# Optimization experiments

Measured on AMD Instinct MI355X. Metric: run time of the kernel, lower is better.

Reference implementation:

```python
import jax, jax.numpy as jnp
import numpy as np
from jax import lax

VOCAB, EMB, HID, NCLS, BATCH, SEQ = 32000, 512, 512, 8, 64, 512


def setup_inputs() -> dict:
    key = jax.random.key(0)
    ks = jax.random.split(key, 12)
    s = 0.05
    return {
        "x": jax.random.randint(ks[0], (BATCH, SEQ), 0, VOCAB),
        "emb": jax.random.normal(ks[1], (VOCAB, EMB), jnp.float32) * s,
        "W_ih0": jax.random.normal(ks[2], (HID, EMB), jnp.float32) * s,
        "W_hh0": jax.random.normal(ks[3], (HID, HID), jnp.float32) * s,
        "b_ih0": jax.random.normal(ks[4], (HID,), jnp.float32) * s,
        "b_hh0": jax.random.normal(ks[5], (HID,), jnp.float32) * s,
        "W_ih1": jax.random.normal(ks[6], (HID, HID), jnp.float32) * s,
        "W_hh1": jax.random.normal(ks[7], (HID, HID), jnp.float32) * s,
        "b_ih1": jax.random.normal(ks[8], (HID,), jnp.float32) * s,
        "b_hh1": jax.random.normal(ks[9], (HID,), jnp.float32) * s,
        "fc_W": jax.random.normal(ks[10], (NCLS, HID), jnp.float32) * s,
        "fc_b": jax.random.normal(ks[11], (NCLS,), jnp.float32) * s,
    }


def _rnn_layer(inp, W_ih, W_hh, b_ih, b_hh):
    # inp: [B, S, F]; tanh RNN, batch_first. Precompute input projection once.
    pre = jnp.einsum('bsf,hf->bsh', inp, W_ih) + b_ih + b_hh  # [B,S,H]
    B = inp.shape[0]
    H = W_hh.shape[0]
    h0 = jnp.zeros((B, H), inp.dtype)

    def step(h, p_t):  # p_t: [B,H]
        h = jnp.tanh(p_t + h @ W_hh.T)
        return h, h

    hT, ys = lax.scan(step, h0, pre.transpose(1, 0, 2))  # scan over time
    return ys.transpose(1, 0, 2), hT  # outputs [B,S,H], last hidden [B,H]


def reference(x, emb, W_ih0, W_hh0, b_ih0, b_hh0, W_ih1, W_hh1, b_ih1, b_hh1, fc_W, fc_b):
    xe = emb[x]  # [B,S,E] embedding lookup
    out0, _ = _rnn_layer(xe, W_ih0, W_hh0, b_ih0, b_hh0)
    _, h1 = _rnn_layer(out0, W_ih1, W_hh1, b_ih1, b_hh1)  # hidden[-1]
    return h1 @ fc_W.T + fc_b  # [B, n_class]
```

## Files before the change

kernel.cpp:

```cpp
#include <hip/hip_runtime.h>
#include <stdint.h>


#define BB 64
#define SS 512
#define HH 512

typedef short bf16x8 __attribute__((ext_vector_type(8)));
typedef float f32x4 __attribute__((ext_vector_type(4)));
typedef int i32x4 __attribute__((ext_vector_type(4)));
typedef unsigned int u32;
typedef u32 u32x2 __attribute__((ext_vector_type(2)));

__device__ __forceinline__ unsigned short f2bf(float f) {
  uint32_t u = __builtin_bit_cast(uint32_t, f);
  u += 0x7FFFu + ((u >> 16) & 1u);
  return (unsigned short)(u >> 16);
}
__device__ __forceinline__ float bf2f(unsigned short h) {
  uint32_t u = ((uint32_t)h) << 16;
  return __builtin_bit_cast(float, u);
}
__device__ __forceinline__ int pack2(unsigned short a, unsigned short b) {
  return (int)(unsigned int)a | ((int)(unsigned int)b << 16);
}
__device__ __forceinline__ u32 hipack(u32 a, u32 b) {
  return (a >> 16) | (b & 0xFFFF0000u);
}
__device__ __forceinline__ u32 lopack(u32 a, u32 b) {
  return (a & 0xFFF8u) | ((b & 0xFFF8u) << 16);
}
__device__ __forceinline__ bool tag4(i32x4 v, u32 t) {
  u32 m = (((u32)v[0] ^ t) | ((u32)v[1] ^ t) | ((u32)v[2] ^ t) | ((u32)v[3] ^ t)) & 7u;
  return m == 0u;
}
__device__ __forceinline__ float fast_tanh(float v) {
  float a = __builtin_fabsf(v);
  float e = __expf(-2.0f * a);
  float t = (1.0f - e) / (1.0f + e);
  return __builtin_copysignf(t, v);
}

#define UC_LOAD4(dst, ptr) \
  asm volatile("global_load_dwordx4 %0, %1, off sc0 sc1" : "=v"(dst) : "v"(ptr))
#define UC_LOAD1(dst, ptr) \
  asm volatile("global_load_dword %0, %1, off sc0 sc1" : "=v"(dst) : "v"(ptr))
#define UC_STORE2(ptr, v) \
  asm volatile("global_store_dwordx2 %0, %1, off sc0 sc1" ::"v"(ptr), "v"(v) : "memory")

__global__ __launch_bounds__(512, 2) void k_rnn(
    const int* __restrict__ x, const float* __restrict__ emb,
    const float* __restrict__ Wih0, const float* __restrict__ Whh0,
    const float* __restrict__ bih0, const float* __restrict__ bhh0,
    const float* __restrict__ Wih1, const float* __restrict__ Whh1,
    const float* __restrict__ bih1, const float* __restrict__ bhh1,
    u32* __restrict__ hsl) {
  const int tid = threadIdx.x;
  const int bid = blockIdx.x;
  const int layer = bid >> 5;
  const int lb = bid & 31;
  const int bg = lb >> 3;
  const int c = lb & 7;
  const int wid = tid >> 6;
  const int lane = tid & 63;
  const int kq = wid >> 1;
  const int nh = wid & 1;

  __shared__ __align__(16) unsigned short s_in0[16 * 512];
  __shared__ __align__(16) unsigned short s_Hhi[16 * 512];
  __shared__ __align__(16) unsigned short s_Hlo[16 * 512];
  __shared__ __align__(16) float s_part[4 * 16 * 64];

  const float* Wih = layer ? Wih1 : Wih0;
  const float* Whh = layer ? Whh1 : Whh0;
  const float* bi = layer ? bih1 : bih0;
  const float* bh = layer ? bhh1 : bhh0;

  bf16x8 wih[2][4], whhh[2][4], whhl[2][4];
  {
    const int r16 = lane & 15, kg = lane >> 4;
#pragma unroll
    for (int nt = 0; nt < 2; ++nt) {
#pragma unroll
      for (int kt = 0; kt < 4; ++kt) {
        int row = c * 64 + nh * 32 + nt * 16 + r16;
        int k0 = kq * 128 + kt * 32 + kg * 8;
        const float* p = Wih + row * 512 + k0;
        bf16x8 v;
#pragma unroll
        for (int j = 0; j < 8; ++j) v[j] = (short)f2bf(p[j]);
        wih[nt][kt] = v;
        const float* q = Whh + row * 512 + k0;
        bf16x8 vh, vl;
#pragma unroll
        for (int j = 0; j < 8; ++j) {
          float f = q[j];
          unsigned short h = f2bf(f);
          vh[j] = (short)h;
          vl[j] = (short)f2bf(f - bf2f(h));
        }
        whhh[nt][kt] = vh;
        whhl[nt][kt] = vl;
      }
    }
  }
  float biasv0, biasv1;
  {
    int na = (tid & 31) * 2;
    biasv0 = bi[c * 64 + na] + bh[c * 64 + na];
    biasv1 = bi[c * 64 + na + 1] + bh[c * 64 + na + 1];
  }

  const int r_st = tid >> 5;
  const int ch = tid & 31;

  float4 pf0, pf1, pf2, pf3;
  if (layer == 0) {
    int rid = x[(bg * 16 + r_st) * SS + 0];
    const float4* ep = (const float4*)(emb + (size_t)rid * 512 + ch * 16);
    pf0 = ep[0]; pf1 = ep[1]; pf2 = ep[2]; pf3 = ep[3];
  }

  for (int s = 1; s <= SS; ++s) {
    const u32 exp_h = (u32)((s - 1) & 7);
    const u32* ph = hsl +
        (((size_t)layer * 4 + ((s - 1) & 3)) * 64 + bg * 16 + r_st) * 512 + ch * 16;

    if (layer == 0) {
      i32x4 v0, v1;
      v0[0] = pack2(f2bf(pf0.x), f2bf(pf0.y));
      v0[1] = pack2(f2bf(pf0.z), f2bf(pf0.w));
      v0[2] = pack2(f2bf(pf1.x), f2bf(pf1.y));
      v0[3] = pack2(f2bf(pf1.z), f2bf(pf1.w));
      v1[0] = pack2(f2bf(pf2.x), f2bf(pf2.y));
      v1[1] = pack2(f2bf(pf2.z), f2bf(pf2.w));
      v1[2] = pack2(f2bf(pf3.x), f2bf(pf3.y));
      v1[3] = pack2(f2bf(pf3.z), f2bf(pf3.w));
      *(i32x4*)(s_in0 + r_st * 512 + (((2 * ch) ^ (r_st & 7)) << 3)) = v0;
      *(i32x4*)(s_in0 + r_st * 512 + (((2 * ch + 1) ^ (r_st & 7)) << 3)) = v1;
      if (s < SS) {
        int rid = x[(bg * 16 + r_st) * SS + s];
        const float4* ep = (const float4*)(emb + (size_t)rid * 512 + ch * 16);
        pf0 = ep[0]; pf1 = ep[1]; pf2 = ep[2]; pf3 = ep[3];
      }
    } else {
      i32x4 i0 = {0, 0, 0, 0}, i1 = {0, 0, 0, 0}, i2 = {0, 0, 0, 0}, i3 = {0, 0, 0, 0};
      const u32 exp_i = (u32)(s & 7);
      const u32* pi =
          hsl + (((size_t)(s & 3)) * 64 + bg * 16 + r_st) * 512 + ch * 16;
      while (true) {
        UC_LOAD4(i0, pi);
        UC_LOAD4(i1, pi + 4);
        UC_LOAD4(i2, pi + 8);
        UC_LOAD4(i3, pi + 12);
        asm volatile("s_waitcnt vmcnt(0)"
                     : "+v"(i0), "+v"(i1), "+v"(i2), "+v"(i3)::"memory");
        bool ok = tag4(i0, exp_i) && tag4(i1, exp_i) && tag4(i2, exp_i) &&
                  tag4(i3, exp_i);
        if (__all(ok)) break;
      }
      i32x4 A0 = {(int)hipack(i0[0], i0[1]), (int)hipack(i0[2], i0[3]),
                  (int)hipack(i1[0], i1[1]), (int)hipack(i1[2], i1[3])};
      i32x4 A1 = {(int)hipack(i2[0], i2[1]), (int)hipack(i2[2], i2[3]),
                  (int)hipack(i3[0], i3[1]), (int)hipack(i3[2], i3[3])};
      *(i32x4*)(s_in0 + r_st * 512 + (((2 * ch) ^ (r_st & 7)) << 3)) = A0;
      *(i32x4*)(s_in0 + r_st * 512 + (((2 * ch + 1) ^ (r_st & 7)) << 3)) = A1;
    }
    __syncthreads();

    f32x4 acc0 = {0.f, 0.f, 0.f, 0.f};
    f32x4 acc1 = {0.f, 0.f, 0.f, 0.f};
    {
      const int r16 = lane & 15, kg = lane >> 4;
#pragma unroll
      for (int kt = 0; kt < 4; ++kt) {
        int k8 = kq * 16 + kt * 4 + kg;
        bf16x8 ain = __builtin_bit_cast(
            bf16x8, *(const i32x4*)(s_in0 + r16 * 512 + ((k8 ^ (r16 & 7)) << 3)));
        acc0 = __builtin_amdgcn_mfma_f32_16x16x32_bf16(ain, wih[0][kt], acc0, 0, 0, 0);
        acc1 = __builtin_amdgcn_mfma_f32_16x16x32_bf16(ain, wih[1][kt], acc1, 0, 0, 0);
      }
    }

    if (s > 1) {
      i32x4 h0 = {0, 0, 0, 0}, h1 = {0, 0, 0, 0}, h2 = {0, 0, 0, 0}, h3 = {0, 0, 0, 0};
      if (layer == 0) {
        const bool need_bp = (s > 4) && (tid < 8);
        const u32 exp_bp = (u32)((s - 4) & 7);
        const u32* pbp = hsl + ((size_t)(4 + ((s - 4) & 3)) * 64 + bg * 16) * 512 +
                         (tid < 8 ? tid * 64 : 0);
        while (true) {
          u32 bpw = 0;
          UC_LOAD4(h0, ph);
          UC_LOAD4(h1, ph + 4);
          UC_LOAD4(h2, ph + 8);
          UC_LOAD4(h3, ph + 12);
          UC_LOAD1(bpw, pbp);
          asm volatile("s_waitcnt vmcnt(0)"
                       : "+v"(h0), "+v"(h1), "+v"(h2), "+v"(h3), "+v"(bpw)::"memory");
          bool ok = tag4(h0, exp_h) && tag4(h1, exp_h) && tag4(h2, exp_h) &&
                    tag4(h3, exp_h) && (!need_bp || ((bpw & 7u) == exp_bp));
          if (__all(ok)) break;
        }
      } else {
        while (true) {
          UC_LOAD4(h0, ph);
          UC_LOAD4(h1, ph + 4);
          UC_LOAD4(h2, ph + 8);
          UC_LOAD4(h3, ph + 12);
          asm volatile("s_waitcnt vmcnt(0)"
                       : "+v"(h0), "+v"(h1), "+v"(h2), "+v"(h3)::"memory");
          bool ok = tag4(h0, exp_h) && tag4(h1, exp_h) && tag4(h2, exp_h) &&
                    tag4(h3, exp_h);
          if (__all(ok)) break;
        }
      }
      i32x4 A0 = {(int)hipack(h0[0], h0[1]), (int)hipack(h0[2], h0[3]),
                  (int)hipack(h1[0], h1[1]), (int)hipack(h1[2], h1[3])};
      i32x4 A1 = {(int)hipack(h2[0], h2[1]), (int)hipack(h2[2], h2[3]),
                  (int)hipack(h3[0], h3[1]), (int)hipack(h3[2], h3[3])};
      i32x4 B0 = {(int)lopack(h0[0], h0[1]), (int)lopack(h0[2], h0[3]),
                  (int)lopack(h1[0], h1[1]), (int)lopack(h1[2], h1[3])};
      i32x4 B1v = {(int)lopack(h2[0], h2[1]), (int)lopack(h2[2], h2[3]),
                   (int)lopack(h3[0], h3[1]), (int)lopack(h3[2], h3[3])};
      *(i32x4*)(s_Hhi + r_st * 512 + (((2 * ch) ^ (r_st & 7)) << 3)) = A0;
      *(i32x4*)(s_Hhi + r_st * 512 + (((2 * ch + 1) ^ (r_st & 7)) << 3)) = A1;
      *(i32x4*)(s_Hlo + r_st * 512 + (((2 * ch) ^ (r_st & 7)) << 3)) = B0;
      *(i32x4*)(s_Hlo + r_st * 512 + (((2 * ch + 1) ^ (r_st & 7)) << 3)) = B1v;
    }
    __syncthreads();

    {
      const int r16 = lane & 15, kg = lane >> 4;
      if (s > 1) {
#pragma unroll
        for (int kt = 0; kt < 4; ++kt) {
          int k8 = kq * 16 + kt * 4 + kg;
          bf16x8 ahi = __builtin_bit_cast(
              bf16x8, *(const i32x4*)(s_Hhi + r16 * 512 + ((k8 ^ (r16 & 7)) << 3)));
          bf16x8 alo = __builtin_bit_cast(
              bf16x8, *(const i32x4*)(s_Hlo + r16 * 512 + ((k8 ^ (r16 & 7)) << 3)));
          acc0 = __builtin_amdgcn_mfma_f32_16x16x32_bf16(ahi, whhh[0][kt], acc0, 0, 0, 0);
          acc0 = __builtin_amdgcn_mfma_f32_16x16x32_bf16(ahi, whhl[0][kt], acc0, 0, 0, 0);
          acc0 = __builtin_amdgcn_mfma_f32_16x16x32_bf16(alo, whhh[0][kt], acc0, 0, 0, 0);
          acc1 = __builtin_amdgcn_mfma_f32_16x16x32_bf16(ahi, whhh[1][kt], acc1, 0, 0, 0);
          acc1 = __builtin_amdgcn_mfma_f32_16x16x32_bf16(ahi, whhl[1][kt], acc1, 0, 0, 0);
          acc1 = __builtin_amdgcn_mfma_f32_16x16x32_bf16(alo, whhh[1][kt], acc1, 0, 0, 0);
        }
      }
#pragma unroll
      for (int j = 0; j < 4; ++j) {
        int m = kg * 4 + j;
        int xr = (m >> 2) & 3;
        int n0i = nh * 32 + 0 * 16 + r16;
        int n1i = nh * 32 + 1 * 16 + r16;
        s_part[kq * 1024 + m * 64 + (n0i ^ (xr << 4))] = acc0[j];
        s_part[kq * 1024 + m * 64 + (n1i ^ (xr << 4))] = acc1[j];
      }
    }
    __syncthreads();

    {
      int m = tid >> 5, na = (tid & 31) * 2;
      int xr = (m >> 2) & 3;
      float v0 = biasv0, v1 = biasv1;
#pragma unroll
      for (int q2 = 0; q2 < 4; ++q2) {
        const float2* sp =
            (const float2*)(s_part + q2 * 1024 + m * 64 + (na ^ (xr << 4)));
        float2 t = *sp;
        v0 += t.x;
        v1 += t.y;
      }
      v0 = fast_tanh(v0);
      v1 = fast_tanh(v1);
      unsigned short a0 = f2bf(v0), a1 = f2bf(v1);
      unsigned short b0 = f2bf(v0 - bf2f(a0)), b1 = f2bf(v1 - bf2f(a1));
      u32 tag = (u32)(s & 7);
      u32x2 wv;
      wv[0] = ((u32)a0 << 16) | ((u32)b0 & 0xFFF8u) | tag;
      wv[1] = ((u32)a1 << 16) | ((u32)b1 & 0xFFF8u) | tag;
      u32* dst = hsl + (((size_t)layer * 4 + (s & 3)) * 64 + bg * 16 + m) * 512 +
                 c * 64 + na;
      UC_STORE2(dst, wv);
    }
  }
}

__global__ void k_fc(const u32* __restrict__ h1w, const float* __restrict__ fcW,
                     const float* __restrict__ fcb, float* __restrict__ out) {
  int i = threadIdx.x;
  int b = i >> 3, cc = i & 7;
  float acc = fcb[cc];
  const u32* ph = h1w + b * 512;
  const float* pw = fcW + cc * 512;
  for (int k = 0; k < 512; k += 4) {
    int4 w4 = *(const int4*)(ph + k);
    float4 wv = *(const float4*)(pw + k);
    acc += (bf2f((unsigned short)((u32)w4.x >> 16)) +
            bf2f((unsigned short)((u32)w4.x & 0xFFF8u))) * wv.x;
    acc += (bf2f((unsigned short)((u32)w4.y >> 16)) +
            bf2f((unsigned short)((u32)w4.y & 0xFFF8u))) * wv.y;
    acc += (bf2f((unsigned short)((u32)w4.z >> 16)) +
            bf2f((unsigned short)((u32)w4.z & 0xFFF8u))) * wv.z;
    acc += (bf2f((unsigned short)((u32)w4.w >> 16)) +
            bf2f((unsigned short)((u32)w4.w & 0xFFF8u))) * wv.w;
  }
  out[b * 8 + cc] = acc;
}

extern "C" void kernel_launch(void* const* d_in, const int* in_sizes, int n_in,
                              void* d_out, int out_size, void* d_ws, size_t ws_size,
                              hipStream_t stream) {
  const int* x = (const int*)d_in[0];
  const float* emb = (const float*)d_in[1];
  const float* Wih0 = (const float*)d_in[2];
  const float* Whh0 = (const float*)d_in[3];
  const float* bih0 = (const float*)d_in[4];
  const float* bhh0 = (const float*)d_in[5];
  const float* Wih1 = (const float*)d_in[6];
  const float* Whh1 = (const float*)d_in[7];
  const float* bih1 = (const float*)d_in[8];
  const float* bhh1 = (const float*)d_in[9];
  const float* fcW = (const float*)d_in[10];
  const float* fcb = (const float*)d_in[11];

  u32* hsl = (u32*)d_ws;

  hipMemsetAsync(hsl, 0, (size_t)2 * 4 * 64 * 512 * 4, stream);
  hipLaunchKernelGGL(k_rnn, dim3(64), dim3(512), 0, stream, x, emb, Wih0, Whh0,
                     bih0, bhh0, Wih1, Whh1, bih1, bhh1, hsl);
  hipLaunchKernelGGL(k_fc, dim3(1), dim3(512), 0, stream,
                     hsl + (size_t)4 * 64 * 512, fcW, fcb, (float*)d_out);
}
```

Measured before the change: 2.071 ms.

## Split input staging and hidden polling across warp halves, drop a barrier

Result: faster. 1.748 ms (-15.6%).

```diff
diff --git a/kernel.cpp b/kernel.cpp
--- a/kernel.cpp
+++ b/kernel.cpp
@@ -48,7 +48,7 @@
 #define UC_STORE2(ptr, v) \
   asm volatile("global_store_dwordx2 %0, %1, off sc0 sc1" ::"v"(ptr), "v"(v) : "memory")
 
-__global__ __launch_bounds__(512, 2) void k_rnn(
+__global__ __launch_bounds__(512, 1) void k_rnn(
     const int* __restrict__ x, const float* __restrict__ emb,
     const float* __restrict__ Wih0, const float* __restrict__ Whh0,
     const float* __restrict__ bih0, const float* __restrict__ bhh0,
@@ -65,6 +65,9 @@
   const int lane = tid & 63;
   const int kq = wid >> 1;
   const int nh = wid & 1;
+  const int gt = tid & 255;
+  const int gr = gt >> 4;
+  const int gch = gt & 15;
 
   __shared__ __align__(16) unsigned short s_in0[16 * 512];
   __shared__ __align__(16) unsigned short s_Hhi[16 * 512];
@@ -111,60 +114,165 @@
     biasv1 = bi[c * 64 + na + 1] + bh[c * 64 + na + 1];
   }
 
-  const int r_st = tid >> 5;
-  const int ch = tid & 31;
-
-  float4 pf0, pf1, pf2, pf3;
-  if (layer == 0) {
-    int rid = x[(bg * 16 + r_st) * SS + 0];
-    const float4* ep = (const float4*)(emb + (size_t)rid * 512 + ch * 16);
-    pf0 = ep[0]; pf1 = ep[1]; pf2 = ep[2]; pf3 = ep[3];
+  float4 pf0, pf1, pf2, pf3, pf4, pf5, pf6, pf7;
+  if (layer == 0 && wid < 4) {
+    int rid = x[(bg * 16 + gr) * SS + 0];
+    const float4* ep = (const float4*)(emb + (size_t)rid * 512);
+    pf0 = ep[2 * gch + 0];  pf1 = ep[2 * gch + 1];
+    pf2 = ep[2 * gch + 32]; pf3 = ep[2 * gch + 33];
+    pf4 = ep[2 * gch + 64]; pf5 = ep[2 * gch + 65];
+    pf6 = ep[2 * gch + 96]; pf7 = ep[2 * gch + 97];
   }
 
   for (int s = 1; s <= SS; ++s) {
     const u32 exp_h = (u32)((s - 1) & 7);
-    const u32* ph = hsl +
-        (((size_t)layer * 4 + ((s - 1) & 3)) * 64 + bg * 16 + r_st) * 512 + ch * 16;
-
-    if (layer == 0) {
-      i32x4 v0, v1;
-      v0[0] = pack2(f2bf(pf0.x), f2bf(pf0.y));
-      v0[1] = pack2(f2bf(pf0.z), f2bf(pf0.w));
-      v0[2] = pack2(f2bf(pf1.x), f2bf(pf1.y));
-      v0[3] = pack2(f2bf(pf1.z), f2bf(pf1.w));
-      v1[0] = pack2(f2bf(pf2.x), f2bf(pf2.y));
-      v1[1] = pack2(f2bf(pf2.z), f2bf(pf2.w));
-      v1[2] = pack2(f2bf(pf3.x), f2bf(pf3.y));
-      v1[3] = pack2(f2bf(pf3.z), f2bf(pf3.w));
-      *(i32x4*)(s_in0 + r_st * 512 + (((2 * ch) ^ (r_st & 7)) << 3)) = v0;
-      *(i32x4*)(s_in0 + r_st * 512 + (((2 * ch + 1) ^ (r_st & 7)) << 3)) = v1;
-      if (s < SS) {
-        int rid = x[(bg * 16 + r_st) * SS + s];
-        const float4* ep = (const float4*)(emb + (size_t)rid * 512 + ch * 16);
-        pf0 = ep[0]; pf1 = ep[1]; pf2 = ep[2]; pf3 = ep[3];
+
+    if (wid < 4) {
+      if (layer == 0) {
+        {
+          i32x4 v;
+          v[0] = pack2(f2bf(pf0.x), f2bf(pf0.y));
+          v[1] = pack2(f2bf(pf0.z), f2bf(pf0.w));
+          v[2] = pack2(f2bf(pf1.x), f2bf(pf1.y));
+          v[3] = pack2(f2bf(pf1.z), f2bf(pf1.w));
+          *(i32x4*)(s_in0 + gr * 512 + (((gch + 0) ^ (gr & 7)) << 3)) = v;
+          v[0] = pack2(f2bf(pf2.x), f2bf(pf2.y));
+          v[1] = pack2(f2bf(pf2.z), f2bf(pf2.w));
+          v[2] = pack2(f2bf(pf3.x), f2bf(pf3.y));
+          v[3] = pack2(f2bf(pf3.z), f2bf(pf3.w));
+          *(i32x4*)(s_in0 + gr * 512 + (((gch + 16) ^ (gr & 7)) << 3)) = v;
+          v[0] = pack2(f2bf(pf4.x), f2bf(pf4.y));
+          v[1] = pack2(f2bf(pf4.z), f2bf(pf4.w));
+          v[2] = pack2(f2bf(pf5.x), f2bf(pf5.y));
+          v[3] = pack2(f2bf(pf5.z), f2bf(pf5.w));
+          *(i32x4*)(s_in0 + gr * 512 + (((gch + 32) ^ (gr & 7)) << 3)) = v;
+          v[0] = pack2(f2bf(pf6.x), f2bf(pf6.y));
+          v[1] = pack2(f2bf(pf6.z), f2bf(pf6.w));
+          v[2] = pack2(f2bf(pf7.x), f2bf(pf7.y));
+          v[3] = pack2(f2bf(pf7.z), f2bf(pf7.w));
+          *(i32x4*)(s_in0 + gr * 512 + (((gch + 48) ^ (gr & 7)) << 3)) = v;
+        }
+        if (s < SS) {
+          int rid = x[(bg * 16 + gr) * SS + s];
+          const float4* ep = (const float4*)(emb + (size_t)rid * 512);
+          pf0 = ep[2 * gch + 0];  pf1 = ep[2 * gch + 1];
+          pf2 = ep[2 * gch + 32]; pf3 = ep[2 * gch + 33];
+          pf4 = ep[2 * gch + 64]; pf5 = ep[2 * gch + 65];
+          pf6 = ep[2 * gch + 96]; pf7 = ep[2 * gch + 97];
+        }
+      } else {
+        i32x4 w0 = {0,0,0,0}, w1 = {0,0,0,0}, w2 = {0,0,0,0}, w3 = {0,0,0,0};
+        i32x4 w4 = {0,0,0,0}, w5 = {0,0,0,0}, w6 = {0,0,0,0}, w7 = {0,0,0,0};
+        const u32 exp_i = (u32)(s & 7);
+        const u32* pib =
+            hsl + (((size_t)(s & 3)) * 64 + bg * 16 + gr) * 512;
+        while (true) {
+          UC_LOAD4(w0, pib + 8 * gch + 0);
+          UC_LOAD4(w1, pib + 8 * gch + 4);
+          UC_LOAD4(w2, pib + 8 * gch + 128);
+          UC_LOAD4(w3, pib + 8 * gch + 132);
+          UC_LOAD4(w4, pib + 8 * gch + 256);
+          UC_LOAD4(w5, pib + 8 * gch + 260);
+          UC_LOAD4(w6, pib + 8 * gch + 384);
+          UC_LOAD4(w7, pib + 8 * gch + 388);
+          asm volatile("s_waitcnt vmcnt(0)"
+                       : "+v"(w0), "+v"(w1), "+v"(w2), "+v"(w3), "+v"(w4),
+                         "+v"(w5), "+v"(w6), "+v"(w7)::"memory");
+          bool ok = tag4(w0, exp_i) && tag4(w1, exp_i) && tag4(w2, exp_i) &&
+                    tag4(w3, exp_i) && tag4(w4, exp_i) && tag4(w5, exp_i) &&
+                    tag4(w6, exp_i) && tag4(w7, exp_i);
+          if (__all(ok)) break;
+        }
+        i32x4 A;
+        A[0] = (int)hipack(w0[0], w0[1]); A[1] = (int)hipack(w0[2], w0[3]);
+        A[2] = (int)hipack(w1[0], w1[1]); A[3] = (int)hipack(w1[2], w1[3]);
+        *(i32x4*)(s_in0 + gr * 512 + (((gch + 0) ^ (gr & 7)) << 3)) = A;
+        A[0] = (int)hipack(w2[0], w2[1]); A[1] = (int)hipack(w2[2], w2[3]);
+        A[2] = (int)hipack(w3[0], w3[1]); A[3] = (int)hipack(w3[2], w3[3]);
+        *(i32x4*)(s_in0 + gr * 512 + (((gch + 16) ^ (gr & 7)) << 3)) = A;
+        A[0] = (int)hipack(w4[0], w4[1]); A[1] = (int)hipack(w4[2], w4[3]);
+        A[2] = (int)hipack(w5[0], w5[1]); A[3] = (int)hipack(w5[2], w5[3]);
+        *(i32x4*)(s_in0 + gr * 512 + (((gch + 32) ^ (gr & 7)) << 3)) = A;
+        A[0] = (int)hipack(w6[0], w6[1]); A[1] = (int)hipack(w6[2], w6[3]);
+        A[2] = (int)hipack(w7[0], w7[1]); A[3] = (int)hipack(w7[2], w7[3]);
+        *(i32x4*)(s_in0 + gr * 512 + (((gch + 48) ^ (gr & 7)) << 3)) = A;
       }
     } else {
-      i32x4 i0 = {0, 0, 0, 0}, i1 = {0, 0, 0, 0}, i2 = {0, 0, 0, 0}, i3 = {0, 0, 0, 0};
-      const u32 exp_i = (u32)(s & 7);
-      const u32* pi =
-          hsl + (((size_t)(s & 3)) * 64 + bg * 16 + r_st) * 512 + ch * 16;
-      while (true) {
-        UC_LOAD4(i0, pi);
-        UC_LOAD4(i1, pi + 4);
-        UC_LOAD4(i2, pi + 8);
-        UC_LOAD4(i3, pi + 12);
-        asm volatile("s_waitcnt vmcnt(0)"
-                     : "+v"(i0), "+v"(i1), "+v"(i2), "+v"(i3)::"memory");
-        bool ok = tag4(i0, exp_i) && tag4(i1, exp_i) && tag4(i2, exp_i) &&
-                  tag4(i3, exp_i);
-        if (__all(ok)) break;
-      }
-      i32x4 A0 = {(int)hipack(i0[0], i0[1]), (int)hipack(i0[2], i0[3]),
-                  (int)hipack(i1[0], i1[1]), (int)hipack(i1[2], i1[3])};
-      i32x4 A1 = {(int)hipack(i2[0], i2[1]), (int)hipack(i2[2], i2[3]),
-                  (int)hipack(i3[0], i3[1]), (int)hipack(i3[2], i3[3])};
-      *(i32x4*)(s_in0 + r_st * 512 + (((2 * ch) ^ (r_st & 7)) << 3)) = A0;
-      *(i32x4*)(s_in0 + r_st * 512 + (((2 * ch + 1) ^ (r_st & 7)) << 3)) = A1;
+      if (s > 1) {
+        i32x4 w0 = {0,0,0,0}, w1 = {0,0,0,0}, w2 = {0,0,0,0}, w3 = {0,0,0,0};
+        i32x4 w4 = {0,0,0,0}, w5 = {0,0,0,0}, w6 = {0,0,0,0}, w7 = {0,0,0,0};
+        const u32* phb = hsl +
+            (((size_t)layer * 4 + ((s - 1) & 3)) * 64 + bg * 16 + gr) * 512;
+        if (layer == 0) {
+          const bool need_bp = (s > 4) && (gt < 8);
+          const u32 exp_bp = (u32)((s - 4) & 7);
+          const u32* pbp = hsl + ((size_t)(4 + ((s - 4) & 3)) * 64 + bg * 16) * 512 +
+                           (gt < 8 ? gt * 64 : 0);
+          while (true) {
+            u32 bpw = 0;
+            UC_LOAD4(w0, phb + 8 * gch + 0);
+            UC_LOAD4(w1, phb + 8 * gch + 4);
+            UC_LOAD4(w2, phb + 8 * gch + 128);
+            UC_LOAD4(w3, phb + 8 * gch + 132);
+            UC_LOAD4(w4, phb + 8 * gch + 256);
+            UC_LOAD4(w5, phb + 8 * gch + 260);
+            UC_LOAD4(w6, phb + 8 * gch + 384);
+            UC_LOAD4(w7, phb + 8 * gch + 388);
+            UC_LOAD1(bpw, pbp);
+            asm volatile("s_waitcnt vmcnt(0)"
+                         : "+v"(w0), "+v"(w1), "+v"(w2), "+v"(w3), "+v"(w4),
+                           "+v"(w5), "+v"(w6), "+v"(w7), "+v"(bpw)::"memory");
+            bool ok = tag4(w0, exp_h) && tag4(w1, exp_h) && tag4(w2, exp_h) &&
+                      tag4(w3, exp_h) && tag4(w4, exp_h) && tag4(w5, exp_h) &&
+                      tag4(w6, exp_h) && tag4(w7, exp_h) &&
+                      (!need_bp || ((bpw & 7u) == exp_bp));
+            if (__all(ok)) break;
+          }
+        } else {
+          while (true) {
+            UC_LOAD4(w0, phb + 8 * gch + 0);
+            UC_LOAD4(w1, phb + 8 * gch + 4);
+            UC_LOAD4(w2, phb + 8 * gch + 128);
+            UC_LOAD4(w3, phb + 8 * gch + 132);
+            UC_LOAD4(w4, phb + 8 * gch + 256);
+            UC_LOAD4(w5, phb + 8 * gch + 260);
+            UC_LOAD4(w6, phb + 8 * gch + 384);
+            UC_LOAD4(w7, phb + 8 * gch + 388);
+            asm volatile("s_waitcnt vmcnt(0)"
+                         : "+v"(w0), "+v"(w1), "+v"(w2), "+v"(w3), "+v"(w4),
+                           "+v"(w5), "+v"(w6), "+v"(w7)::"memory");
+            bool ok = tag4(w0, exp_h) && tag4(w1, exp_h) && tag4(w2, exp_h) &&
+                      tag4(w3, exp_h) && tag4(w4, exp_h) && tag4(w5, exp_h) &&
+                      tag4(w6, exp_h) && tag4(w7, exp_h);
+            if (__all(ok)) break;
+          }
+        }
+        i32x4 A, B;
+        A[0] = (int)hipack(w0[0], w0[1]); A[1] = (int)hipack(w0[2], w0[3]);
+        A[2] = (int)hipack(w1[0], w1[1]); A[3] = (int)hipack(w1[2], w1[3]);
+        B[0] = (int)lopack(w0[0], w0[1]); B[1] = (int)lopack(w0[2], w0[3]);
+        B[2] = (int)lopack(w1[0], w1[1]); B[3] = (int)lopack(w1[2], w1[3]);
+        *(i32x4*)(s_Hhi + gr * 512 + (((gch + 0) ^ (gr & 7)) << 3)) = A;
+        *(i32x4*)(s_Hlo + gr * 512 + (((gch + 0) ^ (gr & 7)) << 3)) = B;
+        A[0] = (int)hipack(w2[0], w2[1]); A[1] = (int)hipack(w2[2], w2[3]);
+        A[2] = (int)hipack(w3[0], w3[1]); A[3] = (int)hipack(w3[2], w3[3]);
+        B[0] = (int)lopack(w2[0], w2[1]); B[1] = (int)lopack(w2[2], w2[3]);
+        B[2] = (int)lopack(w3[0], w3[1]); B[3] = (int)lopack(w3[2], w3[3]);
+        *(i32x4*)(s_Hhi + gr * 512 + (((gch + 16) ^ (gr & 7)) << 3)) = A;
+        *(i32x4*)(s_Hlo + gr * 512 + (((gch + 16) ^ (gr & 7)) << 3)) = B;
+        A[0] = (int)hipack(w4[0], w4[1]); A[1] = (int)hipack(w4[2], w4[3]);
+        A[2] = (int)hipack(w5[0], w5[1]); A[3] = (int)hipack(w5[2], w5[3]);
+        B[0] = (int)lopack(w4[0], w4[1]); B[1] = (int)lopack(w4[2], w4[3]);
+        B[2] = (int)lopack(w5[0], w5[1]); B[3] = (int)lopack(w5[2], w5[3]);
+        *(i32x4*)(s_Hhi + gr * 512 + (((gch + 32) ^ (gr & 7)) << 3)) = A;
+        *(i32x4*)(s_Hlo + gr * 512 + (((gch + 32) ^ (gr & 7)) << 3)) = B;
+        A[0] = (int)hipack(w6[0], w6[1]); A[1] = (int)hipack(w6[2], w6[3]);
+        A[2] = (int)hipack(w7[0], w7[1]); A[3] = (int)hipack(w7[2], w7[3]);
+        B[0] = (int)lopack(w6[0], w6[1]); B[1] = (int)lopack(w6[2], w6[3]);
+        B[2] = (int)lopack(w7[0], w7[1]); B[3] = (int)lopack(w7[2], w7[3]);
+        *(i32x4*)(s_Hhi + gr * 512 + (((gch + 48) ^ (gr & 7)) << 3)) = A;
+        *(i32x4*)(s_Hlo + gr * 512 + (((gch + 48) ^ (gr & 7)) << 3)) = B;
+      }
     }
     __syncthreads();
 
@@ -180,58 +288,6 @@
         acc0 = __builtin_amdgcn_mfma_f32_16x16x32_bf16(ain, wih[0][kt], acc0, 0, 0, 0);
         acc1 = __builtin_amdgcn_mfma_f32_16x16x32_bf16(ain, wih[1][kt], acc1, 0, 0, 0);
       }
-    }
-
-    if (s > 1) {
-      i32x4 h0 = {0, 0, 0, 0}, h1 = {0, 0, 0, 0}, h2 = {0, 0, 0, 0}, h3 = {0, 0, 0, 0};
-      if (layer == 0) {
-        const bool need_bp = (s > 4) && (tid < 8);
-        const u32 exp_bp = (u32)((s - 4) & 7);
-        const u32* pbp = hsl + ((size_t)(4 + ((s - 4) & 3)) * 64 + bg * 16) * 512 +
-                         (tid < 8 ? tid * 64 : 0);
-        while (true) {
-          u32 bpw = 0;
-          UC_LOAD4(h0, ph);
-          UC_LOAD4(h1, ph + 4);
-          UC_LOAD4(h2, ph + 8);
-          UC_LOAD4(h3, ph + 12);
-          UC_LOAD1(bpw, pbp);
-          asm volatile("s_waitcnt vmcnt(0)"
-                       : "+v"(h0), "+v"(h1), "+v"(h2), "+v"(h3), "+v"(bpw)::"memory");
-          bool ok = tag4(h0, exp_h) && tag4(h1, exp_h) && tag4(h2, exp_h) &&
-                    tag4(h3, exp_h) && (!need_bp || ((bpw & 7u) == exp_bp));
-          if (__all(ok)) break;
-        }
-      } else {
-        while (true) {
-          UC_LOAD4(h0, ph);
-          UC_LOAD4(h1, ph + 4);
-          UC_LOAD4(h2, ph + 8);
-          UC_LOAD4(h3, ph + 12);
-          asm volatile("s_waitcnt vmcnt(0)"
-                       : "+v"(h0), "+v"(h1), "+v"(h2), "+v"(h3)::"memory");
-          bool ok = tag4(h0, exp_h) && tag4(h1, exp_h) && tag4(h2, exp_h) &&
-                    tag4(h3, exp_h);
-          if (__all(ok)) break;
-        }
-      }
-      i32x4 A0 = {(int)hipack(h0[0], h0[1]), (int)hipack(h0[2], h0[3]),
-                  (int)hipack(h1[0], h1[1]), (int)hipack(h1[2], h1[3])};
-      i32x4 A1 = {(int)hipack(h2[0], h2[1]), (int)hipack(h2[2], h2[3]),
-                  (int)hipack(h3[0], h3[1]), (int)hipack(h3[2], h3[3])};
-      i32x4 B0 = {(int)lopack(h0[0], h0[1]), (int)lopack(h0[2], h0[3]),
-                  (int)lopack(h1[0], h1[1]), (int)lopack(h1[2], h1[3])};
-      i32x4 B1v = {(int)lopack(h2[0], h2[1]), (int)lopack(h2[2], h2[3]),
-                   (int)lopack(h3[0], h3[1]), (int)lopack(h3[2], h3[3])};
-      *(i32x4*)(s_Hhi + r_st * 512 + (((2 * ch) ^ (r_st & 7)) << 3)) = A0;
-      *(i32x4*)(s_Hhi + r_st * 512 + (((2 * ch + 1) ^ (r_st & 7)) << 3)) = A1;
-      *(i32x4*)(s_Hlo + r_st * 512 + (((2 * ch) ^ (r_st & 7)) << 3)) = B0;
-      *(i32x4*)(s_Hlo + r_st * 512 + (((2 * ch + 1) ^ (r_st & 7)) << 3)) = B1v;
-    }
-    __syncthreads();
-
-    {
-      const int r16 = lane & 15, kg = lane >> 4;
       if (s > 1) {
 #pragma unroll
         for (int kt = 0; kt < 4; ++kt) {
```

## Per-K-quarter hidden-state polling to drop a block barrier in RNN step

Applied to the files above, without the earlier changes.

Measured after the change: 2.343 ms. 13.1% more time.

```diff
diff --git a/kernel.cpp b/kernel.cpp
--- a/kernel.cpp
+++ b/kernel.cpp
@@ -40,6 +40,12 @@
   float t = (1.0f - e) / (1.0f + e);
   return __builtin_copysignf(t, v);
 }
+
+#define BAR_LDS()                                            \
+  do {                                                       \
+    asm volatile("s_waitcnt lgkmcnt(0)" ::: "memory");       \
+    __builtin_amdgcn_s_barrier();                            \
+  } while (0)
 
 #define UC_LOAD4(dst, ptr) \
   asm volatile("global_load_dwordx4 %0, %1, off sc0 sc1" : "=v"(dst) : "v"(ptr))
@@ -48,7 +54,7 @@
 #define UC_STORE2(ptr, v) \
   asm volatile("global_store_dwordx2 %0, %1, off sc0 sc1" ::"v"(ptr), "v"(v) : "memory")
 
-__global__ __launch_bounds__(512, 2) void k_rnn(
+__global__ __launch_bounds__(512, 1) void k_rnn(
     const int* __restrict__ x, const float* __restrict__ emb,
     const float* __restrict__ Wih0, const float* __restrict__ Whh0,
     const float* __restrict__ bih0, const float* __restrict__ bhh0,
@@ -65,10 +71,14 @@
   const int lane = tid & 63;
   const int kq = wid >> 1;
   const int nh = wid & 1;
+  const int lr = lane >> 3;
+  const int lch = lane & 7;
+  const int r_st = tid >> 5;
+  const int ch = tid & 31;
 
   __shared__ __align__(16) unsigned short s_in0[16 * 512];
-  __shared__ __align__(16) unsigned short s_Hhi[16 * 512];
-  __shared__ __align__(16) unsigned short s_Hlo[16 * 512];
+  __shared__ __align__(16) unsigned short s_Hq_hi[4 * 16 * 128];
+  __shared__ __align__(16) unsigned short s_Hq_lo[4 * 16 * 128];
   __shared__ __align__(16) float s_part[4 * 16 * 64];
 
   const float* Wih = layer ? Wih1 : Wih0;
@@ -111,9 +121,6 @@
     biasv1 = bi[c * 64 + na + 1] + bh[c * 64 + na + 1];
   }
 
-  const int r_st = tid >> 5;
-  const int ch = tid & 31;
-
   float4 pf0, pf1, pf2, pf3;
   if (layer == 0) {
     int rid = x[(bg * 16 + r_st) * SS + 0];
@@ -123,8 +130,6 @@
 
   for (int s = 1; s <= SS; ++s) {
     const u32 exp_h = (u32)((s - 1) & 7);
-    const u32* ph = hsl +
-        (((size_t)layer * 4 + ((s - 1) & 3)) * 64 + bg * 16 + r_st) * 512 + ch * 16;
 
     if (layer == 0) {
       i32x4 v0, v1;
@@ -144,7 +149,8 @@
         pf0 = ep[0]; pf1 = ep[1]; pf2 = ep[2]; pf3 = ep[3];
       }
     } else {
-      i32x4 i0 = {0, 0, 0, 0}, i1 = {0, 0, 0, 0}, i2 = {0, 0, 0, 0}, i3 = {0, 0, 0, 0};
+      i32x4 i0 = {0, 0, 0, 0}, i1 = {0, 0, 0, 0}, i2 = {0, 0, 0, 0},
+            i3 = {0, 0, 0, 0};
       const u32 exp_i = (u32)(s & 7);
       const u32* pi =
           hsl + (((size_t)(s & 3)) * 64 + bg * 16 + r_st) * 512 + ch * 16;
@@ -166,7 +172,7 @@
       *(i32x4*)(s_in0 + r_st * 512 + (((2 * ch) ^ (r_st & 7)) << 3)) = A0;
       *(i32x4*)(s_in0 + r_st * 512 + (((2 * ch + 1) ^ (r_st & 7)) << 3)) = A1;
     }
-    __syncthreads();
+    BAR_LDS();
 
     f32x4 acc0 = {0.f, 0.f, 0.f, 0.f};
     f32x4 acc1 = {0.f, 0.f, 0.f, 0.f};
@@ -183,63 +189,77 @@
     }
 
     if (s > 1) {
-      i32x4 h0 = {0, 0, 0, 0}, h1 = {0, 0, 0, 0}, h2 = {0, 0, 0, 0}, h3 = {0, 0, 0, 0};
-      if (layer == 0) {
-        const bool need_bp = (s > 4) && (tid < 8);
-        const u32 exp_bp = (u32)((s - 4) & 7);
-        const u32* pbp = hsl + ((size_t)(4 + ((s - 4) & 3)) * 64 + bg * 16) * 512 +
-                         (tid < 8 ? tid * 64 : 0);
-        while (true) {
-          u32 bpw = 0;
-          UC_LOAD4(h0, ph);
-          UC_LOAD4(h1, ph + 4);
-          UC_LOAD4(h2, ph + 8);
-          UC_LOAD4(h3, ph + 12);
-          UC_LOAD1(bpw, pbp);
-          asm volatile("s_waitcnt vmcnt(0)"
-                       : "+v"(h0), "+v"(h1), "+v"(h2), "+v"(h3), "+v"(bpw)::"memory");
-          bool ok = tag4(h0, exp_h) && tag4(h1, exp_h) && tag4(h2, exp_h) &&
-                    tag4(h3, exp_h) && (!need_bp || ((bpw & 7u) == exp_bp));
-          if (__all(ok)) break;
-        }
-      } else {
-        while (true) {
-          UC_LOAD4(h0, ph);
-          UC_LOAD4(h1, ph + 4);
-          UC_LOAD4(h2, ph + 8);
-          UC_LOAD4(h3, ph + 12);
-          asm volatile("s_waitcnt vmcnt(0)"
-                       : "+v"(h0), "+v"(h1), "+v"(h2), "+v"(h3)::"memory");
-          bool ok = tag4(h0, exp_h) && tag4(h1, exp_h) && tag4(h2, exp_h) &&
-                    tag4(h3, exp_h);
-          if (__all(ok)) break;
-        }
-      }
-      i32x4 A0 = {(int)hipack(h0[0], h0[1]), (int)hipack(h0[2], h0[3]),
-                  (int)hipack(h1[0], h1[1]), (int)hipack(h1[2], h1[3])};
-      i32x4 A1 = {(int)hipack(h2[0], h2[1]), (int)hipack(h2[2], h2[3]),
-                  (int)hipack(h3[0], h3[1]), (int)hipack(h3[2], h3[3])};
-      i32x4 B0 = {(int)lopack(h0[0], h0[1]), (int)lopack(h0[2], h0[3]),
-                  (int)lopack(h1[0], h1[1]), (int)lopack(h1[2], h1[3])};
-      i32x4 B1v = {(int)lopack(h2[0], h2[1]), (int)lopack(h2[2], h2[3]),
-                   (int)lopack(h3[0], h3[1]), (int)lopack(h3[2], h3[3])};
-      *(i32x4*)(s_Hhi + r_st * 512 + (((2 * ch) ^ (r_st & 7)) << 3)) = A0;
-      *(i32x4*)(s_Hhi + r_st * 512 + (((2 * ch + 1) ^ (r_st & 7)) << 3)) = A1;
-      *(i32x4*)(s_Hlo + r_st * 512 + (((2 * ch) ^ (r_st & 7)) << 3)) = B0;
-      *(i32x4*)(s_Hlo + r_st * 512 + (((2 * ch + 1) ^ (r_st & 7)) << 3)) = B1v;
-    }
-    __syncthreads();
-
-    {
-      const int r16 = lane & 15, kg = lane >> 4;
-      if (s > 1) {
+      i32x4 w0 = {0,0,0,0}, w1 = {0,0,0,0}, w2 = {0,0,0,0}, w3 = {0,0,0,0};
+      i32x4 w4 = {0,0,0,0}, w5 = {0,0,0,0}, w6 = {0,0,0,0}, w7 = {0,0,0,0};
+      const u32* pq = hsl +
+          (((size_t)layer * 4 + ((s - 1) & 3)) * 64 + bg * 16) * 512 + kq * 128;
+      const u32* pA = pq + lr * 512 + lch * 16;
+      const u32* pB = pA + 8 * 512;
+      const bool bp_wave = (layer == 0) && (wid == 0) && (s > 4);
+      const u32 exp_bp = (u32)((s - 4) & 7);
+      const u32* pbp = hsl + ((size_t)(4 + ((s - 4) & 3)) * 64 + bg * 16) * 512 +
+                       (lane < 8 ? lane * 64 : 0);
+      while (true) {
+        u32 bw = 0;
+        UC_LOAD4(w0, pA);
+        UC_LOAD4(w1, pA + 4);
+        UC_LOAD4(w2, pA + 8);
+        UC_LOAD4(w3, pA + 12);
+        UC_LOAD4(w4, pB);
+        UC_LOAD4(w5, pB + 4);
+        UC_LOAD4(w6, pB + 8);
+        UC_LOAD4(w7, pB + 12);
+        if (bp_wave) UC_LOAD1(bw, pbp);
+        asm volatile("s_waitcnt vmcnt(0)"
+                     : "+v"(w0), "+v"(w1), "+v"(w2), "+v"(w3), "+v"(w4),
+                       "+v"(w5), "+v"(w6), "+v"(w7), "+v"(bw)::"memory");
+        bool ok = tag4(w0, exp_h) && tag4(w1, exp_h) && tag4(w2, exp_h) &&
+                  tag4(w3, exp_h) && tag4(w4, exp_h) && tag4(w5, exp_h) &&
+                  tag4(w6, exp_h) && tag4(w7, exp_h) &&
+                  (!bp_wave || lane >= 8 || ((bw & 7u) == exp_bp));
+        if (__all(ok)) break;
+      }
+      {
+        const int c0 = lch * 2;
+        unsigned short* bh_ = s_Hq_hi + kq * 2048 + lr * 128;
+        unsigned short* bl_ = s_Hq_lo + kq * 2048 + lr * 128;
+        i32x4 T;
+        T[0] = (int)hipack(w0[0], w0[1]); T[1] = (int)hipack(w0[2], w0[3]);
+        T[2] = (int)hipack(w1[0], w1[1]); T[3] = (int)hipack(w1[2], w1[3]);
+        *(i32x4*)(bh_ + (((c0 + 0) ^ (lr & 7)) << 3)) = T;
+        T[0] = (int)hipack(w2[0], w2[1]); T[1] = (int)hipack(w2[2], w2[3]);
+        T[2] = (int)hipack(w3[0], w3[1]); T[3] = (int)hipack(w3[2], w3[3]);
+        *(i32x4*)(bh_ + (((c0 + 1) ^ (lr & 7)) << 3)) = T;
+        T[0] = (int)lopack(w0[0], w0[1]); T[1] = (int)lopack(w0[2], w0[3]);
+        T[2] = (int)lopack(w1[0], w1[1]); T[3] = (int)lopack(w1[2], w1[3]);
+        *(i32x4*)(bl_ + (((c0 + 0) ^ (lr & 7)) << 3)) = T;
+        T[0] = (int)lopack(w2[0], w2[1]); T[1] = (int)lopack(w2[2], w2[3]);
+        T[2] = (int)lopack(w3[0], w3[1]); T[3] = (int)lopack(w3[2], w3[3]);
+        *(i32x4*)(bl_ + (((c0 + 1) ^ (lr & 7)) << 3)) = T;
+        unsigned short* bh2 = bh_ + 8 * 128;
+        unsigned short* bl2 = bl_ + 8 * 128;
+        T[0] = (int)hipack(w4[0], w4[1]); T[1] = (int)hipack(w4[2], w4[3]);
+        T[2] = (int)hipack(w5[0], w5[1]); T[3] = (int)hipack(w5[2], w5[3]);
+        *(i32x4*)(bh2 + (((c0 + 0) ^ (lr & 7)) << 3)) = T;
+        T[0] = (int)hipack(w6[0], w6[1]); T[1] = (int)hipack(w6[2], w6[3]);
+        T[2] = (int)hipack(w7[0], w7[1]); T[3] = (int)hipack(w7[2], w7[3]);
+        *(i32x4*)(bh2 + (((c0 + 1) ^ (lr & 7)) << 3)) = T;
+        T[0] = (int)lopack(w4[0], w4[1]); T[1] = (int)lopack(w4[2], w4[3]);
+        T[2] = (int)lopack(w5[0], w5[1]); T[3] = (int)lopack(w5[2], w5[3]);
+        *(i32x4*)(bl2 + (((c0 + 0) ^ (lr & 7)) << 3)) = T;
+        T[0] = (int)lopack(w6[0], w6[1]); T[1] = (int)lopack(w6[2], w6[3]);
+        T[2] = (int)lopack(w7[0], w7[1]); T[3] = (int)lopack(w7[2], w7[3]);
+        *(i32x4*)(bl2 + (((c0 + 1) ^ (lr & 7)) << 3)) = T;
+      }
+      {
+        const int r16 = lane & 15, kg = lane >> 4;
 #pragma unroll
         for (int kt = 0; kt < 4; ++kt) {
-          int k8 = kq * 16 + kt * 4 + kg;
+          const int cidx = ((kt * 4 + kg) ^ (r16 & 7)) << 3;
           bf16x8 ahi = __builtin_bit_cast(
-              bf16x8, *(const i32x4*)(s_Hhi + r16 * 512 + ((k8 ^ (r16 & 7)) << 3)));
+              bf16x8, *(const i32x4*)(s_Hq_hi + kq * 2048 + r16 * 128 + cidx));
           bf16x8 alo = __builtin_bit_cast(
-              bf16x8, *(const i32x4*)(s_Hlo + r16 * 512 + ((k8 ^ (r16 & 7)) << 3)));
+              bf16x8, *(const i32x4*)(s_Hq_lo + kq * 2048 + r16 * 128 + cidx));
           acc0 = __builtin_amdgcn_mfma_f32_16x16x32_bf16(ahi, whhh[0][kt], acc0, 0, 0, 0);
           acc0 = __builtin_amdgcn_mfma_f32_16x16x32_bf16(ahi, whhl[0][kt], acc0, 0, 0, 0);
           acc0 = __builtin_amdgcn_mfma_f32_16x16x32_bf16(alo, whhh[0][kt], acc0, 0, 0, 0);
@@ -248,6 +268,10 @@
           acc1 = __builtin_amdgcn_mfma_f32_16x16x32_bf16(alo, whhh[1][kt], acc1, 0, 0, 0);
         }
       }
+    }
+
+    {
+      const int r16 = lane & 15, kg = lane >> 4;
 #pragma unroll
       for (int j = 0; j < 4; ++j) {
         int m = kg * 4 + j;
@@ -258,7 +282,7 @@
         s_part[kq * 1024 + m * 64 + (n1i ^ (xr << 4))] = acc1[j];
       }
     }
-    __syncthreads();
+    BAR_LDS();
 
     {
       int m = tid >> 5, na = (tid & 31) * 2;
```
